# Kernel tuning notes

Hardware: AMD Instinct MI355X
Metric: run time of the kernel (lower is better)

The kernel has to match this reference:

```python
import jax, jax.numpy as jnp
from jax import lax
import numpy as np

B, H, W = 2, 48, 48
C_IN, C_OUT = 96, 192
D_INNER, N_STATE, DT_RANK, K = 192, 16, 6, 4  # VMamba: expand=2, d_state=16, dt_rank=ceil(C/16)
EPS = 1e-5


def setup_inputs() -> dict:
    ks = jax.random.split(jax.random.key(0), 16)
    s = 0.02
    r = lambda k, sh, sc=s: jax.random.normal(k, sh, jnp.float32) * sc
    d, N, R = D_INNER, N_STATE, DT_RANK
    return {
        "x": jax.random.normal(ks[0], (B, C_IN, H, W), jnp.float32),
        "ln_g": jnp.ones((C_IN,), jnp.float32),
        "ln_b": jnp.zeros((C_IN,), jnp.float32),
        "in_proj_w": r(ks[1], (2 * d, C_IN)),
        "dwconv_w": r(ks[2], (d, 1, 3, 3)),
        "dwconv_b": jnp.zeros((d,), jnp.float32),
        "x_proj_w": r(ks[3], (K, R + 2 * N, d)),
        "dt_w": r(ks[4], (K, d, R)),
        "dt_b": r(ks[5], (K, d), 0.1),
        "A_logs": jnp.tile(jnp.log(jnp.arange(1, N + 1, dtype=jnp.float32)), (K, d, 1)),
        "Ds": jnp.ones((K, d), jnp.float32),
        "out_norm_g": jnp.ones((d,), jnp.float32),
        "out_norm_b": jnp.zeros((d,), jnp.float32),
        "out_proj_w": r(ks[6], (C_IN, d)),
        "w1": r(ks[7], (C_OUT, C_IN, 1, 1)),
        "b1": jnp.zeros((C_OUT,), jnp.float32),
        "w31": r(ks[8], (C_OUT, C_IN, 3, 3)),
        "b31": jnp.zeros((C_OUT,), jnp.float32),
        "w32": r(ks[9], (C_OUT, C_IN, 3, 3)),
        "b32": jnp.zeros((C_OUT,), jnp.float32),
        "w33": r(ks[10], (C_OUT, C_OUT, 3, 3)),
        "b33": jnp.zeros((C_OUT,), jnp.float32),
        "bn_g": jnp.ones((3 * C_OUT,), jnp.float32),
        "bn_b": jnp.zeros((3 * C_OUT,), jnp.float32),
        "bn_m": r(ks[11], (3 * C_OUT,), 0.1),
        "bn_v": jax.random.uniform(ks[12], (3 * C_OUT,), jnp.float32) + 0.5,
        "prelu_a": jnp.float32(0.25),
    }


def _layernorm(x, g, b):
    m = jnp.mean(x, -1, keepdims=True)
    v = jnp.var(x, -1, keepdims=True)
    return (x - m) * lax.rsqrt(v + EPS) * g + b


def _conv(x, w, b, stride, pad, groups=1):
    y = lax.conv_general_dilated(x, w, (stride, stride), [(pad, pad), (pad, pad)],
                                 dimension_numbers=("NCHW", "OIHW", "NCHW"),
                                 feature_group_count=groups)
    return y + b[None, :, None, None]


def _ss2d(x, in_proj_w, dwconv_w, dwconv_b, x_proj_w, dt_w, dt_b, A_logs, Ds,
          out_norm_g, out_norm_b, out_proj_w):
    # x: (B, H, W, C)
    Bb, Hh, Ww, C = x.shape
    d, N, R = D_INNER, N_STATE, DT_RANK
    L = Hh * Ww
    xz = jnp.einsum("bhwc,ec->bhwe", x, in_proj_w)  # (B,H,W,2d)
    xin, z = jnp.split(xz, 2, axis=-1)
    xc = jnp.transpose(xin, (0, 3, 1, 2))           # (B,d,H,W)
    xc = jax.nn.silu(_conv(xc, dwconv_w, dwconv_b, 1, 1, groups=d))
    # 4 scan directions: row-major, col-major, and their reverses
    x_flat = xc.reshape(Bb, d, L)
    x_t = jnp.transpose(xc, (0, 1, 3, 2)).reshape(Bb, d, L)
    xs = jnp.stack([x_flat, x_t, x_flat[:, :, ::-1], x_t[:, :, ::-1]], axis=1)  # (B,K,d,L)
    x_dbl = jnp.einsum("bkdl,kcd->bkcl", xs, x_proj_w)
    dts, Bs, Cs = x_dbl[:, :, :R], x_dbl[:, :, R:R + N], x_dbl[:, :, R + N:]
    delta = jax.nn.softplus(jnp.einsum("bkrl,kdr->bkdl", dts, dt_w) + dt_b[None, :, :, None])
    A = -jnp.exp(A_logs)                                   # (K,d,N)
    dA = jnp.exp(jnp.einsum("bkdl,kdn->lbkdn", delta, A))  # (L,B,K,d,N)
    dBu = jnp.einsum("bkdl,bknl,bkdl->lbkdn", delta, Bs, xs)
    Cseq = jnp.transpose(Cs, (3, 0, 1, 2))                 # (L,B,K,N)

    def step(h, inp):
        dA_t, dBu_t, c_t = inp
        h = dA_t * h + dBu_t
        return h, jnp.einsum("bkdn,bkn->bkd", h, c_t)

    h0 = jnp.zeros((Bb, K, d, N), x.dtype)
    _, ys = lax.scan(step, h0, (dA, dBu, Cseq))            # ys: (L,B,K,d)
    ys = jnp.transpose(ys, (1, 2, 3, 0)) + xs * Ds[None, :, :, None]  # (B,K,d,L)

    def t_back(a):  # undo the HW transpose of col-major scans
        return jnp.transpose(a.reshape(Bb, d, Ww, Hh), (0, 1, 3, 2)).reshape(Bb, d, L)

    y = ys[:, 0] + ys[:, 2, :, ::-1] + t_back(ys[:, 1]) + t_back(ys[:, 3, :, ::-1])
    y = _layernorm(jnp.transpose(y, (0, 2, 1)), out_norm_g, out_norm_b).reshape(Bb, Hh, Ww, d)
    y = y * jax.nn.silu(z)
    return jnp.einsum("bhwd,cd->bhwc", y, out_proj_w)


def reference(x, ln_g, ln_b, in_proj_w, dwconv_w, dwconv_b, x_proj_w, dt_w, dt_b,
              A_logs, Ds, out_norm_g, out_norm_b, out_proj_w,
              w1, b1, w31, b31, w32, b32, w33, b33,
              bn_g, bn_b, bn_m, bn_v, prelu_a):
    # VSSBlock: residual + SS2D on LayerNorm'd NHWC features
    x_nhwc = jnp.transpose(x, (0, 2, 3, 1))
    x_nhwc = x_nhwc + _ss2d(_layernorm(x_nhwc, ln_g, ln_b), in_proj_w, dwconv_w,
                            dwconv_b, x_proj_w, dt_w, dt_b, A_logs, Ds,
                            out_norm_g, out_norm_b, out_proj_w)
    xm = jnp.transpose(x_nhwc, (0, 3, 1, 2))  # (B,C,H,W)
    # multi-branch stride-2 downsample
    x1 = _conv(xm, w1, b1, 2, 0)
    x2 = _conv(xm, w31, b31, 2, 1)
    x3 = _conv(_conv(xm, w32, b32, 2, 1), w33, b33, 1, 1)
    out = jnp.concatenate([x1, x2, x3], axis=1)  # (B, 3*C_OUT, H/2, W/2)
    # BatchNorm2d (inference, running stats) + PReLU(single param)
    out = (out - bn_m[None, :, None, None]) * lax.rsqrt(bn_v + EPS)[None, :, None, None] \
          * bn_g[None, :, None, None] + bn_b[None, :, None, None]
    return jnp.where(out > 0, out, prelu_a * out)
```

## Files before the change

### kernel.cpp

```cpp
#include <hip/hip_runtime.h>
#include <math.h>

#define BB_ 2
#define HH 48
#define WW 48
#define LL 2304
#define CIN 96
#define DD 192
#define KK 4
#define NN 16
#define RR 6
#define NCH 64
#define LC 36
#define COUT 192
#define OH 24
#define OW 24
#define OHW 576
#define NPX 1152
#define NTOT 4608
#define EPSF 1e-5f

__global__ __launch_bounds__(256) void k_prep(const float* __restrict__ x,
                                              const float* __restrict__ g,
                                              const float* __restrict__ b,
                                              const float* __restrict__ inw,
                                              const float* __restrict__ xpw,
                                              const float* __restrict__ w31,
                                              const float* __restrict__ w32,
                                              const float* __restrict__ w33,
                                              const float* __restrict__ w1,
                                              const float* __restrict__ wout,
                                              float* __restrict__ stats,
                                              float* __restrict__ WgT,
                                              float* __restrict__ sWg,
                                              float* __restrict__ sWb,
                                              float* __restrict__ At3,
                                              float* __restrict__ At1,
                                              float* __restrict__ At2,
                                              float* __restrict__ woutT) {
  int bx = blockIdx.x;
  int tid = threadIdx.x;
  if (bx < 72) {
    int bb = bx / 36; int l0 = (bx % 36) * 64;
    int p = tid >> 2, q = tid & 3;
    int l = l0 + p;
    const float* xp = x + bb * CIN * LL + l;
    float s = 0.f, ss = 0.f;
    for (int c = q; c < CIN; c += 4) { float v = xp[c * LL]; s += v; ss += v * v; }
    s += __shfl_xor(s, 1, 64); s += __shfl_xor(s, 2, 64);
    ss += __shfl_xor(ss, 1, 64); ss += __shfl_xor(ss, 2, 64);
    if (q == 0) {
      float m = s / CIN; float var = ss / CIN - m * m;
      stats[(bb * LL + l) * 2 + 0] = m;
      stats[(bb * LL + l) * 2 + 1] = rsqrtf(var + EPSF);
    }
  } else if (bx == 72) {
    for (int e = tid; e < 2 * DD; e += 256) {
      float swg = 0.f, swb = 0.f;
      for (int c = 0; c < CIN; c++) {
        float w = inw[e * CIN + c];
        float wg = w * g[c];
        WgT[c * 384 + e] = wg;
        swg += wg; swb += w * b[c];
      }
      sWg[e] = swg; sWb[e] = swb;
    }
  } else if (bx < 217) {
    int idx = (bx - 73) * 256 + tid;
    if (idx < 192 * 192) {
      int m = idx % 192, d = idx / 192;
      At3[idx] = (m < 152) ? xpw[m * 192 + d] : 0.f;
    }
  } else if (bx < 2161) {
    int i = (bx - 217) * 256 + tid;
    if (i < 864 * 576) {
      int k = i / 576, m = i % 576;
      float v;
      if (m < 192) v = w31[m * 864 + k];
      else if (m < 384) v = w32[(m - 192) * 864 + k];
      else v = (k % 9 == 4) ? w1[(m - 384) * 96 + k / 9] : 0.f;
      At1[i] = v;
    }
  } else if (bx < 3457) {
    int i = (bx - 2161) * 256 + tid;
    if (i < 1728 * 192) {
      int k = i / 192, m = i % 192;
      At2[i] = w33[m * 1728 + k];
    }
  } else {
    int i = (bx - 3457) * 256 + tid;
    if (i < 192 * 128) {
      int d = i / 128, e = i % 128;
      woutT[i] = (e < 96) ? wout[e * 192 + d] : 0.f;
    }
  }
}

__global__ __launch_bounds__(256) void k_dwconv(const float* __restrict__ xin,
                                                const float* __restrict__ wdw,
                                                const float* __restrict__ bdw,
                                                float* __restrict__ xs,
                                                float* __restrict__ xsl) {
  __shared__ float vt[32 * 50];
  int bid = blockIdx.x;
  int bb = bid / 288; int r = bid % 288; int dg = r / 72; int tile = r % 72;
  int l0 = tile * 32;
  int d0 = dg * 48;
  for (int i = threadIdx.x; i < 32 * 48; i += 256) {
    int lj = i & 31, dl = i >> 5;
    int d = d0 + dl;
    int l = l0 + lj;
    int h = l / WW, w = l % WW;
    const float* xp = xin + (bb * DD + d) * LL;
    const float* wq = wdw + d * 9;
    float acc = bdw[d];
#pragma unroll
    for (int kh = 0; kh < 3; kh++) {
      int ih = h + kh - 1; if (ih < 0 || ih >= HH) continue;
#pragma unroll
      for (int kw = 0; kw < 3; kw++) {
        int iw = w + kw - 1; if (iw < 0 || iw >= WW) continue;
        acc += xp[ih * WW + iw] * wq[kh * 3 + kw];
      }
    }
    float v = acc / (1.f + __expf(-acc));
    vt[lj * 50 + dl] = v;
    xsl[(size_t)d * NTOT + bb * LL + l] = v;
  }
  __syncthreads();
  for (int j = threadIdx.x; j < 32 * 48; j += 256) {
    int lj = j / 48, dl = j - lj * 48;
    int d = d0 + dl;
    int l = l0 + lj;
    int h = l / WW, w = l % WW;
    int lt = w * HH + h;
    float v = vt[lj * 50 + dl];
    xs[(((size_t)bb * KK + 0) * LL + l) * DD + d] = v;
    xs[(((size_t)bb * KK + 1) * LL + lt) * DD + d] = v;
    xs[(((size_t)bb * KK + 2) * LL + (LL - 1 - l)) * DD + d] = v;
    xs[(((size_t)bb * KK + 3) * LL + (LL - 1 - lt)) * DD + d] = v;
  }
}

__global__ __launch_bounds__(256) void k_dtsplit(const float* __restrict__ C1,
                                                 const float* __restrict__ dtw,
                                                 const float* __restrict__ dtb,
                                                 float* __restrict__ Bsb,
                                                 float* __restrict__ Csb,
                                                 float* __restrict__ delta) {
  __shared__ float lds[38 * 33];
  int bid = blockIdx.x;
  int tile = bid % 72; int bk = bid / 72; int bb = bk >> 2; int k = bk & 3;
  int l0 = tile * 32;
  int tid = threadIdx.x;
  for (int i = tid; i < 38 * 32; i += 256) {
    int r = i >> 5, lj = i & 31;
    lds[r * 33 + lj] = C1[(size_t)(k * 38 + r) * NTOT + bb * LL + l0 + lj];
  }
  __syncthreads();
  for (int i = tid; i < 32 * 16; i += 256) {
    int lj = i >> 4, n = i & 15;
    int l = l0 + lj; int h = l / WW, w = l % WW; int lt = w * HH + h;
    int pos = (k == 0) ? l : (k == 1) ? lt : (k == 2) ? (LL - 1 - l) : (LL - 1 - lt);
    size_t base = ((size_t)bk * LL + pos) * NN + n;
    Bsb[base] = lds[(6 + n) * 33 + lj];
    Csb[base] = lds[(22 + n) * 33 + lj];
  }
  for (int i = tid; i < 32 * 192; i += 256) {
    int lj = i / 192, d = i - lj * 192;
    int l = l0 + lj; int h = l / WW, w = l % WW; int lt = w * HH + h;
    int pos = (k == 0) ? l : (k == 1) ? lt : (k == 2) ? (LL - 1 - l) : (LL - 1 - lt);
    const float* wd = dtw + (k * DD + d) * RR;
    float acc = dtb[k * DD + d];
#pragma unroll
    for (int r = 0; r < RR; r++) acc += wd[r] * lds[r * 33 + lj];
    float sp = acc > 20.f ? acc : log1pf(__expf(acc));
    delta[((size_t)bk * LL + pos) * DD + d] = sp;
  }
}

__global__ __launch_bounds__(192) void k_scan1(const float* __restrict__ delta,
                                               const float* __restrict__ xs,
                                               const float* __restrict__ Bsb,
                                               const float* __restrict__ A_logs,
                                               float* __restrict__ Pbuf,
                                               float* __restrict__ Sbuf) {
  __shared__ float Bls[LC * NN];
  int bid = blockIdx.x;
  int c = bid & (NCH - 1); int bk = bid >> 6; int k = bk & 3;
  int t0 = c * LC;
  int d = threadIdx.x;
  const float* bp = Bsb + ((size_t)bk * LL + t0) * NN;
  for (int i = d; i < LC * NN; i += 192) Bls[i] = bp[i];
  float A[NN];
  {
    const float4* ap = (const float4*)(A_logs + (k * DD + d) * NN);
#pragma unroll
    for (int j = 0; j < 4; j++) {
      float4 a4 = ap[j];
      A[4 * j + 0] = -__expf(a4.x); A[4 * j + 1] = -__expf(a4.y);
      A[4 * j + 2] = -__expf(a4.z); A[4 * j + 3] = -__expf(a4.w);
    }
  }
  bool seq = true;
#pragma unroll
  for (int n = 0; n < NN; n++) seq = seq && (fabsf(A[n] + (float)(n + 1)) < 1e-3f);
  float h[NN];
#pragma unroll
  for (int n = 0; n < NN; n++) h[n] = 0.f;
  float sd = 0.f;
  __syncthreads();
  const float* dp = delta + ((size_t)bk * LL + t0) * DD + d;
  const float* xp = xs + ((size_t)bk * LL + t0) * DD + d;
#pragma unroll 2
  for (int t = 0; t < LC; ++t) {
    float dt = dp[t * DD];
    float xv = xp[t * DD];
    float u = dt * xv;
    sd += dt;
    float dA[NN];
    if (seq) {
      float q = __expf(-dt);
      dA[0] = q;
#pragma unroll
      for (int n = 1; n < NN; n++) dA[n] = dA[n - 1] * q;
    } else {
#pragma unroll
      for (int n = 0; n < NN; n++) dA[n] = __expf(dt * A[n]);
    }
    const float4* b4 = (const float4*)&Bls[t * NN];
#pragma unroll
    for (int j = 0; j < 4; j++) {
      float4 bv = b4[j];
      h[4 * j + 0] = dA[4 * j + 0] * h[4 * j + 0] + u * bv.x;
      h[4 * j + 1] = dA[4 * j + 1] * h[4 * j + 1] + u * bv.y;
      h[4 * j + 2] = dA[4 * j + 2] * h[4 * j + 2] + u * bv.z;
      h[4 * j + 3] = dA[4 * j + 3] * h[4 * j + 3] + u * bv.w;
    }
  }
  int chn = (bk * DD + d) * NN;
  float* pp = Pbuf + (size_t)c * 24576 + chn;
  float* sp = Sbuf + (size_t)c * 24576 + chn;
#pragma unroll
  for (int n = 0; n < NN; n++) { pp[n] = __expf(A[n] * sd); sp[n] = h[n]; }
}

__global__ __launch_bounds__(256) void k_scan2(const float* __restrict__ Pbuf,
                                               const float* __restrict__ Sbuf,
                                               float* __restrict__ Hinit) {
  int idx = blockIdx.x * 256 + threadIdx.x;
  float h = 0.f;
  for (int c = 0; c < NCH; c++) {
    Hinit[(size_t)c * 24576 + idx] = h;
    h = Pbuf[(size_t)c * 24576 + idx] * h + Sbuf[(size_t)c * 24576 + idx];
  }
}

__global__ __launch_bounds__(192) void k_scan3(const float* __restrict__ delta,
                                               const float* __restrict__ xs,
                                               const float* __restrict__ Bsb,
                                               const float* __restrict__ Csb,
                                               const float* __restrict__ A_logs,
                                               const float* __restrict__ Ds,
                                               const float* __restrict__ Hinit,
                                               float* __restrict__ ys) {
  __shared__ float Bls[LC * NN];
  __shared__ float Cls[LC * NN];
  int bid = blockIdx.x;
  int c = bid & (NCH - 1); int bk = bid >> 6; int k = bk & 3;
  int t0 = c * LC;
  int d = threadIdx.x;
  const float* bp = Bsb + ((size_t)bk * LL + t0) * NN;
  const float* cp = Csb + ((size_t)bk * LL + t0) * NN;
  for (int i = d; i < LC * NN; i += 192) { Bls[i] = bp[i]; Cls[i] = cp[i]; }
  float A[NN];
  {
    const float4* ap = (const float4*)(A_logs + (k * DD + d) * NN);
#pragma unroll
    for (int j = 0; j < 4; j++) {
      float4 a4 = ap[j];
      A[4 * j + 0] = -__expf(a4.x); A[4 * j + 1] = -__expf(a4.y);
      A[4 * j + 2] = -__expf(a4.z); A[4 * j + 3] = -__expf(a4.w);
    }
  }
  bool seq = true;
#pragma unroll
  for (int n = 0; n < NN; n++) seq = seq && (fabsf(A[n] + (float)(n + 1)) < 1e-3f);
  float Dv = Ds[k * DD + d];
  float h[NN];
  {
    const float4* hp = (const float4*)(Hinit + (size_t)c * 24576 + (bk * DD + d) * NN);
#pragma unroll
    for (int j = 0; j < 4; j++) {
      float4 h4 = hp[j];
      h[4 * j + 0] = h4.x; h[4 * j + 1] = h4.y;
      h[4 * j + 2] = h4.z; h[4 * j + 3] = h4.w;
    }
  }
  __syncthreads();
  const float* dp = delta + ((size_t)bk * LL + t0) * DD + d;
  const float* xp = xs + ((size_t)bk * LL + t0) * DD + d;
  float* yp = ys + ((size_t)bk * LL + t0) * DD + d;
#pragma unroll 2
  for (int t = 0; t < LC; ++t) {
    float dt = dp[t * DD];
    float xv = xp[t * DD];
    float u = dt * xv;
    float y = 0.f;
    float dA[NN];
    if (seq) {
      float q = __expf(-dt);
      dA[0] = q;
#pragma unroll
      for (int n = 1; n < NN; n++) dA[n] = dA[n - 1] * q;
    } else {
#pragma unroll
      for (int n = 0; n < NN; n++) dA[n] = __expf(dt * A[n]);
    }
    const float4* b4 = (const float4*)&Bls[t * NN];
    const float4* c4 = (const float4*)&Cls[t * NN];
#pragma unroll
    for (int j = 0; j < 4; j++) {
      float4 bv = b4[j];
      float4 cc = c4[j];
      h[4 * j + 0] = dA[4 * j + 0] * h[4 * j + 0] + u * bv.x;
      h[4 * j + 1] = dA[4 * j + 1] * h[4 * j + 1] + u * bv.y;
      h[4 * j + 2] = dA[4 * j + 2] * h[4 * j + 2] + u * bv.z;
      h[4 * j + 3] = dA[4 * j + 3] * h[4 * j + 3] + u * bv.w;
      y += h[4 * j + 0] * cc.x + h[4 * j + 1] * cc.y
         + h[4 * j + 2] * cc.z + h[4 * j + 3] * cc.w;
    }
    yp[t * DD] = y + Dv * xv;
  }
}

__global__ __launch_bounds__(256) void k_combine(const float* __restrict__ ys,
                                                 const float* __restrict__ z,
                                                 const float* __restrict__ ong,
                                                 const float* __restrict__ onb,
                                                 float* __restrict__ ya) {
  __shared__ float yt[32 * 193];
  int bx = blockIdx.x; int bb = bx / 72; int l0 = (bx % 72) * 32;
  int tid = threadIdx.x;
  for (int i = tid; i < 32 * DD; i += 256) {
    int p = i / DD, d = i - p * DD;
    int l = l0 + p; int h = l / WW, w = l - h * WW;
    int t1 = w * HH + h;
    float v = ys[(((size_t)bb * KK + 0) * LL + l) * DD + d]
            + ys[(((size_t)bb * KK + 1) * LL + t1) * DD + d]
            + ys[(((size_t)bb * KK + 2) * LL + (LL - 1 - l)) * DD + d]
            + ys[(((size_t)bb * KK + 3) * LL + (LL - 1 - t1)) * DD + d];
    yt[p * 193 + d] = v;
  }
  __syncthreads();
  int p = tid >> 3, q = tid & 7;
  int l = l0 + p;
  float s = 0.f, ss = 0.f;
  for (int d = q * 24; d < q * 24 + 24; d++) { float v = yt[p * 193 + d]; s += v; ss += v * v; }
  s += __shfl_xor(s, 1, 64); s += __shfl_xor(s, 2, 64); s += __shfl_xor(s, 4, 64);
  ss += __shfl_xor(ss, 1, 64); ss += __shfl_xor(ss, 2, 64); ss += __shfl_xor(ss, 4, 64);
  float m = s / DD, var = ss / DD - m * m;
  float rr = rsqrtf(var + EPSF);
  const float* zp = z + (bb * LL + l) * DD;
  for (int d = q * 24; d < q * 24 + 24; d++) {
    float v = (yt[p * 193 + d] - m) * rr * ong[d] + onb[d];
    float zv = zp[d];
    yt[p * 193 + d] = v * zv / (1.f + __expf(-zv));
  }
  __syncthreads();
  for (int i = tid; i < 32 * DD; i += 256) {
    int d = i >> 5, p2 = i & 31;
    ya[(bb * DD + d) * LL + l0 + p2] = yt[p2 * 193 + d];
  }
}

__global__ __launch_bounds__(256) void k_pack1(const float* __restrict__ xm,
                                               float* __restrict__ Bm1) {
  int idx4 = blockIdx.x * 256 + threadIdx.x;
  if (idx4 >= 864 * 288) return;
  int k = idx4 / 288; int n = (idx4 % 288) * 4;
  int ci = k / 9, r9 = k % 9, kh = r9 / 3, kw = r9 % 3;
  int bb = n / OHW, rem = n % OHW, oh = rem / OW, ow0 = rem % OW;
  int ih = 2 * oh + kh - 1;
  float4 v = {0.f, 0.f, 0.f, 0.f};
  if (ih >= 0 && ih < HH) {
    const float* base = xm + (bb * CIN + ci) * LL + ih * WW;
    int iw0 = 2 * ow0 + kw - 1;
    v.x = (iw0 >= 0) ? base[iw0] : 0.f;
    v.y = base[iw0 + 2];
    v.z = base[iw0 + 4];
    v.w = base[iw0 + 6];
  }
  *(float4*)&Bm1[k * NPX + n] = v;
}

__global__ __launch_bounds__(256) void k_pack2(const float* __restrict__ t3,
                                               float* __restrict__ Bm2) {
  int idx4 = blockIdx.x * 256 + threadIdx.x;
  if (idx4 >= 1728 * 288) return;
  int k = idx4 / 288; int n = (idx4 % 288) * 4;
  int ci = k / 9, r9 = k % 9, kh = r9 / 3, kw = r9 % 3;
  int bb = n / OHW, rem = n % OHW, oh = rem / OW, ow0 = rem % OW;
  int ih = oh + kh - 1;
  float4 v = {0.f, 0.f, 0.f, 0.f};
  if (ih >= 0 && ih < OH) {
    const float* base = t3 + (bb * COUT + ci) * OHW + ih * OW;
    int iw0 = ow0 + kw - 1;
    v.x = (iw0 >= 0) ? base[iw0] : 0.f;
    v.y = base[iw0 + 1];
    v.z = base[iw0 + 2];
    v.w = (iw0 + 3 < OW) ? base[iw0 + 3] : 0.f;
  }
  *(float4*)&Bm2[k * NPX + n] = v;
}

template<int MT, int KCHUNK, int NB>
__global__ __launch_bounds__(256) void k_gemm(const float* __restrict__ At,
                                              const float* __restrict__ Bm,
                                              float* __restrict__ Cout) {
  __shared__ float As[16][64];
  __shared__ float Bs[16][64];
  int n0 = blockIdx.x * 64;
  int m0 = blockIdx.y * 64;
  int kz = blockIdx.z;
  int k0 = kz * KCHUNK;
  int tid = threadIdx.x;
  int lr = tid >> 4;
  int lc = (tid & 15) * 4;
  int tm = tid >> 4;
  int tn = tid & 15;
  float acc[4][4] = {};
  for (int ks = 0; ks < KCHUNK; ks += 16) {
    int kg = k0 + ks + lr;
    *(float4*)&As[lr][lc] = *(const float4*)&At[kg * MT + m0 + lc];
    *(float4*)&Bs[lr][lc] = *(const float4*)&Bm[(size_t)kg * NB + n0 + lc];
    __syncthreads();
#pragma unroll
    for (int kk = 0; kk < 16; kk++) {
      float4 a = *(float4*)&As[kk][tm * 4];
      float4 b = *(float4*)&Bs[kk][tn * 4];
      acc[0][0] += a.x * b.x; acc[0][1] += a.x * b.y; acc[0][2] += a.x * b.z; acc[0][3] += a.x * b.w;
      acc[1][0] += a.y * b.x; acc[1][1] += a.y * b.y; acc[1][2] += a.y * b.z; acc[1][3] += a.y * b.w;
      acc[2][0] += a.z * b.x; acc[2][1] += a.z * b.y; acc[2][2] += a.z * b.z; acc[2][3] += a.z * b.w;
      acc[3][0] += a.w * b.x; acc[3][1] += a.w * b.y; acc[3][2] += a.w * b.z; acc[3][3] += a.w * b.w;
    }
    __syncthreads();
  }
  float* cp = Cout + ((size_t)kz * MT + m0) * NB + n0;
#pragma unroll
  for (int i = 0; i < 4; i++) {
    float4 v = {acc[i][0], acc[i][1], acc[i][2], acc[i][3]};
    *(float4*)&cp[(size_t)(tm * 4 + i) * NB + tn * 4] = v;
  }
}

template<int MT, int KD, int EPI>
__global__ __launch_bounds__(256) void k_gemmF(const float* __restrict__ At,
                                               const float* __restrict__ Bm,
                                               int ldb, int boffB,
                                               float* __restrict__ C0,
                                               int ldc, int boffC,
                                               const float* __restrict__ a0,
                                               const float* __restrict__ a1,
                                               const float* __restrict__ a2,
                                               float* __restrict__ a3) {
  __shared__ float As[16][64];
  __shared__ float Bs[16][64];
  int n0 = blockIdx.x * 64;
  int m0 = blockIdx.y * 64;
  int bb = blockIdx.z;
  const float* B = Bm + (size_t)bb * boffB;
  int tid = threadIdx.x;
  int lr = tid >> 4;
  int lc = (tid & 15) * 4;
  int tm = tid >> 4;
  int tn = tid & 15;
  float acc[4][4] = {};
  for (int ks = 0; ks < KD; ks += 16) {
    *(float4*)&As[lr][lc] = *(const float4*)&At[(ks + lr) * MT + m0 + lc];
    *(float4*)&Bs[lr][lc] = *(const float4*)&B[(size_t)(ks + lr) * ldb + n0 + lc];
    __syncthreads();
#pragma unroll
    for (int kk = 0; kk < 16; kk++) {
      float4 a = *(float4*)&As[kk][tm * 4];
      float4 b = *(float4*)&Bs[kk][tn * 4];
      acc[0][0] += a.x * b.x; acc[0][1] += a.x * b.y; acc[0][2] += a.x * b.z; acc[0][3] += a.x * b.w;
      acc[1][0] += a.y * b.x; acc[1][1] += a.y * b.y; acc[1][2] += a.y * b.z; acc[1][3] += a.y * b.w;
      acc[2][0] += a.z * b.x; acc[2][1] += a.z * b.y; acc[2][2] += a.z * b.z; acc[2][3] += a.z * b.w;
      acc[3][0] += a.w * b.x; acc[3][1] += a.w * b.y; acc[3][2] += a.w * b.z; acc[3][3] += a.w * b.w;
    }
    __syncthreads();
  }
  int n = n0 + tn * 4;
  if (EPI == 2) {
    float m_[4], r_[4];
#pragma unroll
    for (int j = 0; j < 4; j++) {
      m_[j] = a0[((size_t)bb * LL + n + j) * 2];
      r_[j] = a0[((size_t)bb * LL + n + j) * 2 + 1];
    }
#pragma unroll
    for (int i = 0; i < 4; i++) {
      int e = m0 + tm * 4 + i;
      float swg = a1[e], swb = a2[e];
      float v0 = r_[0] * (acc[i][0] - m_[0] * swg) + swb;
      float v1 = r_[1] * (acc[i][1] - m_[1] * swg) + swb;
      float v2 = r_[2] * (acc[i][2] - m_[2] * swg) + swb;
      float v3 = r_[3] * (acc[i][3] - m_[3] * swg) + swb;
      if (e < DD) {
        float4 v = {v0, v1, v2, v3};
        *(float4*)&C0[(size_t)bb * boffC + (size_t)e * ldc + n] = v;
      } else {
        a3[((size_t)bb * LL + n + 0) * DD + (e - DD)] = v0;
        a3[((size_t)bb * LL + n + 1) * DD + (e - DD)] = v1;
        a3[((size_t)bb * LL + n + 2) * DD + (e - DD)] = v2;
        a3[((size_t)bb * LL + n + 3) * DD + (e - DD)] = v3;
      }
    }
  } else {
#pragma unroll
    for (int i = 0; i < 4; i++) {
      int e = m0 + tm * 4 + i;
      if (e < CIN) {
        size_t off = (size_t)bb * boffC + (size_t)e * ldc + n;
        float4 xr = *(const float4*)&a0[off];
        float4 v = {acc[i][0] + xr.x, acc[i][1] + xr.y, acc[i][2] + xr.z, acc[i][3] + xr.w};
        *(float4*)&C0[off] = v;
      }
    }
  }
}

__global__ __launch_bounds__(256) void k_reduce1(const float* __restrict__ Cp1,
                                                 const float* __restrict__ b1,
                                                 const float* __restrict__ b31,
                                                 const float* __restrict__ b32,
                                                 const float* __restrict__ bn_g,
                                                 const float* __restrict__ bn_b,
                                                 const float* __restrict__ bn_m,
                                                 const float* __restrict__ bn_v,
                                                 const float* __restrict__ prelu_a,
                                                 float* __restrict__ out,
                                                 float* __restrict__ t3) {
  int idx = blockIdx.x * 256 + threadIdx.x;
  if (idx >= 576 * NPX) return;
  int m = idx / NPX, n = idx % NPX;
  float s = 0.f;
#pragma unroll
  for (int c = 0; c < 6; c++) s += Cp1[(size_t)c * 576 * NPX + idx];
  int bb = n / OHW, o = n % OHW;
  if (m < 192) {
    s += b31[m];
    int cc = 192 + m;
    float scale = rsqrtf(bn_v[cc] + EPSF) * bn_g[cc];
    float v = s * scale + (bn_b[cc] - bn_m[cc] * scale);
    float a = prelu_a[0];
    out[((size_t)bb * 576 + cc) * OHW + o] = v > 0.f ? v : a * v;
  } else if (m < 384) {
    s += b32[m - 192];
    t3[((size_t)bb * COUT + (m - 192)) * OHW + o] = s;
  } else {
    s += b1[m - 384];
    int cc = m - 384;
    float scale = rsqrtf(bn_v[cc] + EPSF) * bn_g[cc];
    float v = s * scale + (bn_b[cc] - bn_m[cc] * scale);
    float a = prelu_a[0];
    out[((size_t)bb * 576 + cc) * OHW + o] = v > 0.f ? v : a * v;
  }
}

__global__ __launch_bounds__(256) void k_reduce2(const float* __restrict__ Cp2,
                                                 const float* __restrict__ b33,
                                                 const float* __restrict__ bn_g,
                                                 const float* __restrict__ bn_b,
                                                 const float* __restrict__ bn_m,
                                                 const float* __restrict__ bn_v,
                                                 const float* __restrict__ prelu_a,
                                                 float* __restrict__ out) {
  int idx = blockIdx.x * 256 + threadIdx.x;
  if (idx >= 192 * NPX) return;
  int m = idx / NPX, n = idx % NPX;
  float s = b33[m];
#pragma unroll
  for (int c = 0; c < 9; c++) s += Cp2[(size_t)c * 192 * NPX + idx];
  int bb = n / OHW, o = n % OHW;
  int cc = 384 + m;
  float scale = rsqrtf(bn_v[cc] + EPSF) * bn_g[cc];
  float v = s * scale + (bn_b[cc] - bn_m[cc] * scale);
  float a = prelu_a[0];
  out[((size_t)bb * 576 + cc) * OHW + o] = v > 0.f ? v : a * v;
}

extern "C" void kernel_launch(void* const* d_in, const int* in_sizes, int n_in,
                              void* d_out, int out_size, void* d_ws, size_t ws_size,
                              hipStream_t stream) {
  const float* x        = (const float*)d_in[0];
  const float* ln_g     = (const float*)d_in[1];
  const float* ln_b     = (const float*)d_in[2];
  const float* in_proj_w= (const float*)d_in[3];
  const float* dwconv_w = (const float*)d_in[4];
  const float* dwconv_b = (const float*)d_in[5];
  const float* x_proj_w = (const float*)d_in[6];
  const float* dt_w     = (const float*)d_in[7];
  const float* dt_b     = (const float*)d_in[8];
  const float* A_logs   = (const float*)d_in[9];
  const float* Ds       = (const float*)d_in[10];
  const float* out_norm_g = (const float*)d_in[11];
  const float* out_norm_b = (const float*)d_in[12];
  const float* out_proj_w = (const float*)d_in[13];
  const float* w1  = (const float*)d_in[14];
  const float* b1  = (const float*)d_in[15];
  const float* w31 = (const float*)d_in[16];
  const float* b31 = (const float*)d_in[17];
  const float* w32 = (const float*)d_in[18];
  const float* b32 = (const float*)d_in[19];
  const float* w33 = (const float*)d_in[20];
  const float* b33 = (const float*)d_in[21];
  const float* bn_g = (const float*)d_in[22];
  const float* bn_b = (const float*)d_in[23];
  const float* bn_m = (const float*)d_in[24];
  const float* bn_v = (const float*)d_in[25];
  const float* prelu_a = (const float*)d_in[26];

  float* ws = (float*)d_ws;
  float* stats = ws + 0;
  float* WgT   = ws + 16384;
  float* sWg   = ws + 65536;
  float* sWb   = ws + 66048;
  float* At3   = ws + 98304;
  float* At1   = ws + 147456;
  float* At2   = ws + 655360;
  float* woutT = ws + 1048576;
  float* xin   = ws + 2097152;
  float* z     = ws + 3145728;
  float* xs    = ws + 4194304;
  float* xsl   = ws + 8388608;
  float* C1    = ws + 9437184;
  float* delta = ws + 10485760;
  float* Bsb   = ws + 14155776;
  float* Csb   = ws + 14680064;
  float* Pbuf  = ws + 15728640;
  float* Sbuf  = ws + 17301504;
  float* Hinit = ws + 18874368;
  float* ys    = ws + 20971520;
  float* ya    = ws + 25165824;
  float* xm    = ws + 26214400;
  float* t3    = ws + 27262976;
  float* Bm1   = ws + 28311552;
  float* Bm2   = ws + 29360128;
  float* Cp1   = ws + 31457280;
  float* Cp2   = ws + 35651584;
  float* out = (float*)d_out;

  k_prep<<<3553, 256, 0, stream>>>(x, ln_g, ln_b, in_proj_w, x_proj_w,
                                   w31, w32, w33, w1, out_proj_w,
                                   stats, WgT, sWg, sWb, At3, At1, At2, woutT);
  k_gemmF<384, 96, 2><<<dim3(36, 6, 2), 256, 0, stream>>>(
      WgT, x, LL, CIN * LL, xin, LL, DD * LL, stats, sWg, sWb, z);
  k_dwconv<<<576, 256, 0, stream>>>(xin, dwconv_w, dwconv_b, xs, xsl);
  k_gemm<192, 192, NTOT><<<dim3(72, 3, 1), 256, 0, stream>>>(At3, xsl, C1);
  k_dtsplit<<<576, 256, 0, stream>>>(C1, dt_w, dt_b, Bsb, Csb, delta);
  k_scan1<<<512, 192, 0, stream>>>(delta, xs, Bsb, A_logs, Pbuf, Sbuf);
  k_scan2<<<96, 256, 0, stream>>>(Pbuf, Sbuf, Hinit);
  k_scan3<<<512, 192, 0, stream>>>(delta, xs, Bsb, Csb, A_logs, Ds, Hinit, ys);
  k_combine<<<144, 256, 0, stream>>>(ys, z, out_norm_g, out_norm_b, ya);
  k_gemmF<128, 192, 3><<<dim3(36, 2, 2), 256, 0, stream>>>(
      woutT, ya, LL, DD * LL, xm, LL, CIN * LL, x, nullptr, nullptr, nullptr);
  k_pack1<<<972, 256, 0, stream>>>(xm, Bm1);
  k_gemm<576, 144, NPX><<<dim3(18, 9, 6), 256, 0, stream>>>(At1, Bm1, Cp1);
  k_reduce1<<<2592, 256, 0, stream>>>(Cp1, b1, b31, b32, bn_g, bn_b, bn_m, bn_v,
                                      prelu_a, out, t3);
  k_pack2<<<1944, 256, 0, stream>>>(t3, Bm2);
  k_gemm<192, 192, NPX><<<dim3(18, 3, 9), 256, 0, stream>>>(At2, Bm2, Cp2);
  k_reduce2<<<864, 256, 0, stream>>>(Cp2, b33, bn_g, bn_b, bn_m, bn_v, prelu_a, out);
}
```

Baseline: 205.9 us.

## Fuse im2col into conv GEMMs, tile weight transposes, dedupe scan inputs

The explicit im2col pack kernels are removed. The conv GEMMs now gather input patches straight from the feature maps while loading their B tiles, which saves two launches and a large staging buffer round trip. The weight transposes in the prep kernel now go through shared-memory 32x32 tiles so both reads and writes are coalesced. The dwconv kernel stores only two scan-direction copies of xs instead of four, and the scans read the reversed directions with a negative stride. The cost is uncoalesced, bounds-checked gathers inside the GEMM inner loop.

```diff
diff --git a/kernel.cpp b/kernel.cpp
--- a/kernel.cpp
+++ b/kernel.cpp
@@ -38,6 +38,7 @@
                                               float* __restrict__ At1,
                                               float* __restrict__ At2,
                                               float* __restrict__ woutT) {
+  __shared__ float tile[32][33];
   int bx = blockIdx.x;
   int tid = threadIdx.x;
   if (bx < 72) {
@@ -65,30 +66,41 @@
       }
       sWg[e] = swg; sWb[e] = swb;
     }
-  } else if (bx < 217) {
+  } else if (bx < 218) {
     int idx = (bx - 73) * 256 + tid;
     if (idx < 192 * 192) {
       int m = idx % 192, d = idx / 192;
       At3[idx] = (m < 152) ? xpw[m * 192 + d] : 0.f;
     }
-  } else if (bx < 2161) {
-    int i = (bx - 217) * 256 + tid;
-    if (i < 864 * 576) {
-      int k = i / 576, m = i % 576;
-      float v;
-      if (m < 192) v = w31[m * 864 + k];
-      else if (m < 384) v = w32[(m - 192) * 864 + k];
-      else v = (k % 9 == 4) ? w1[(m - 384) * 96 + k / 9] : 0.f;
-      At1[i] = v;
-    }
-  } else if (bx < 3457) {
-    int i = (bx - 2161) * 256 + tid;
-    if (i < 1728 * 192) {
+  } else if (bx < 542) {
+    int tt = bx - 218;
+    const float* srcw = (tt < 162) ? w31 : w32;
+    int mofs = (tt < 162) ? 0 : 192;
+    if (tt >= 162) tt -= 162;
+    int kt = tt / 6, mt = tt % 6;
+    int r = tid >> 5, c = tid & 31;
+    for (int rr = r; rr < 32; rr += 8)
+      tile[rr][c] = srcw[(mt * 32 + rr) * 864 + kt * 32 + c];
+    __syncthreads();
+    for (int rr = r; rr < 32; rr += 8)
+      At1[(kt * 32 + rr) * 576 + mofs + mt * 32 + c] = tile[c][rr];
+  } else if (bx < 1190) {
+    int i = (bx - 542) * 256 + tid;
+    if (i < 864 * 192) {
       int k = i / 192, m = i % 192;
-      At2[i] = w33[m * 1728 + k];
-    }
+      At1[k * 576 + 384 + m] = (k % 9 == 4) ? w1[m * 96 + k / 9] : 0.f;
+    }
+  } else if (bx < 1514) {
+    int tt = bx - 1190;
+    int kt = tt / 6, mt = tt % 6;
+    int r = tid >> 5, c = tid & 31;
+    for (int rr = r; rr < 32; rr += 8)
+      tile[rr][c] = w33[(mt * 32 + rr) * 1728 + kt * 32 + c];
+    __syncthreads();
+    for (int rr = r; rr < 32; rr += 8)
+      At2[(kt * 32 + rr) * 192 + mt * 32 + c] = tile[c][rr];
   } else {
-    int i = (bx - 3457) * 256 + tid;
+    int i = (bx - 1514) * 256 + tid;
     if (i < 192 * 128) {
       int d = i / 128, e = i % 128;
       woutT[i] = (e < 96) ? wout[e * 192 + d] : 0.f;
@@ -135,10 +147,8 @@
     int h = l / WW, w = l % WW;
     int lt = w * HH + h;
     float v = vt[lj * 50 + dl];
-    xs[(((size_t)bb * KK + 0) * LL + l) * DD + d] = v;
-    xs[(((size_t)bb * KK + 1) * LL + lt) * DD + d] = v;
-    xs[(((size_t)bb * KK + 2) * LL + (LL - 1 - l)) * DD + d] = v;
-    xs[(((size_t)bb * KK + 3) * LL + (LL - 1 - lt)) * DD + d] = v;
+    xs[((size_t)(bb * 2 + 0) * LL + l) * DD + d] = v;
+    xs[((size_t)(bb * 2 + 1) * LL + lt) * DD + d] = v;
   }
 }
 
@@ -187,7 +197,7 @@
                                                float* __restrict__ Sbuf) {
   __shared__ float Bls[LC * NN];
   int bid = blockIdx.x;
-  int c = bid & (NCH - 1); int bk = bid >> 6; int k = bk & 3;
+  int c = bid & (NCH - 1); int bk = bid >> 6; int k = bk & 3; int bb = bk >> 2;
   int t0 = c * LC;
   int d = threadIdx.x;
   const float* bp = Bsb + ((size_t)bk * LL + t0) * NN;
@@ -211,11 +221,14 @@
   float sd = 0.f;
   __syncthreads();
   const float* dp = delta + ((size_t)bk * LL + t0) * DD + d;
-  const float* xp = xs + ((size_t)bk * LL + t0) * DD + d;
+  const float* xpb = xs + ((size_t)(bb * 2 + (k & 1)) * LL) * DD + d;
+  const float* xp; int xstep;
+  if (k < 2) { xp = xpb + (size_t)t0 * DD; xstep = DD; }
+  else       { xp = xpb + (size_t)(LL - 1 - t0) * DD; xstep = -DD; }
 #pragma unroll 2
   for (int t = 0; t < LC; ++t) {
     float dt = dp[t * DD];
-    float xv = xp[t * DD];
+    float xv = xp[t * xstep];
     float u = dt * xv;
     sd += dt;
     float dA[NN];
@@ -267,7 +280,7 @@
   __shared__ float Bls[LC * NN];
   __shared__ float Cls[LC * NN];
   int bid = blockIdx.x;
-  int c = bid & (NCH - 1); int bk = bid >> 6; int k = bk & 3;
+  int c = bid & (NCH - 1); int bk = bid >> 6; int k = bk & 3; int bb = bk >> 2;
   int t0 = c * LC;
   int d = threadIdx.x;
   const float* bp = Bsb + ((size_t)bk * LL + t0) * NN;
@@ -299,12 +312,15 @@
   }
   __syncthreads();
   const float* dp = delta + ((size_t)bk * LL + t0) * DD + d;
-  const float* xp = xs + ((size_t)bk * LL + t0) * DD + d;
+  const float* xpb = xs + ((size_t)(bb * 2 + (k & 1)) * LL) * DD + d;
+  const float* xp; int xstep;
+  if (k < 2) { xp = xpb + (size_t)t0 * DD; xstep = DD; }
+  else       { xp = xpb + (size_t)(LL - 1 - t0) * DD; xstep = -DD; }
   float* yp = ys + ((size_t)bk * LL + t0) * DD + d;
 #pragma unroll 2
   for (int t = 0; t < LC; ++t) {
     float dt = dp[t * DD];
-    float xv = xp[t * DD];
+    float xv = xp[t * xstep];
     float u = dt * xv;
     float y = 0.f;
     float dA[NN];
@@ -372,46 +388,6 @@
     int d = i >> 5, p2 = i & 31;
     ya[(bb * DD + d) * LL + l0 + p2] = yt[p2 * 193 + d];
   }
-}
-
-__global__ __launch_bounds__(256) void k_pack1(const float* __restrict__ xm,
-                                               float* __restrict__ Bm1) {
-  int idx4 = blockIdx.x * 256 + threadIdx.x;
-  if (idx4 >= 864 * 288) return;
-  int k = idx4 / 288; int n = (idx4 % 288) * 4;
-  int ci = k / 9, r9 = k % 9, kh = r9 / 3, kw = r9 % 3;
-  int bb = n / OHW, rem = n % OHW, oh = rem / OW, ow0 = rem % OW;
-  int ih = 2 * oh + kh - 1;
-  float4 v = {0.f, 0.f, 0.f, 0.f};
-  if (ih >= 0 && ih < HH) {
-    const float* base = xm + (bb * CIN + ci) * LL + ih * WW;
-    int iw0 = 2 * ow0 + kw - 1;
-    v.x = (iw0 >= 0) ? base[iw0] : 0.f;
-    v.y = base[iw0 + 2];
-    v.z = base[iw0 + 4];
-    v.w = base[iw0 + 6];
-  }
-  *(float4*)&Bm1[k * NPX + n] = v;
-}
-
-__global__ __launch_bounds__(256) void k_pack2(const float* __restrict__ t3,
-                                               float* __restrict__ Bm2) {
-  int idx4 = blockIdx.x * 256 + threadIdx.x;
-  if (idx4 >= 1728 * 288) return;
-  int k = idx4 / 288; int n = (idx4 % 288) * 4;
-  int ci = k / 9, r9 = k % 9, kh = r9 / 3, kw = r9 % 3;
-  int bb = n / OHW, rem = n % OHW, oh = rem / OW, ow0 = rem % OW;
-  int ih = oh + kh - 1;
-  float4 v = {0.f, 0.f, 0.f, 0.f};
-  if (ih >= 0 && ih < OH) {
-    const float* base = t3 + (bb * COUT + ci) * OHW + ih * OW;
-    int iw0 = ow0 + kw - 1;
-    v.x = (iw0 >= 0) ? base[iw0] : 0.f;
-    v.y = base[iw0 + 1];
-    v.z = base[iw0 + 2];
-    v.w = (iw0 + 3 < OW) ? base[iw0 + 3] : 0.f;
-  }
-  *(float4*)&Bm2[k * NPX + n] = v;
 }
 
 template<int MT, int KCHUNK, int NB>
@@ -451,6 +427,61 @@
   for (int i = 0; i < 4; i++) {
     float4 v = {acc[i][0], acc[i][1], acc[i][2], acc[i][3]};
     *(float4*)&cp[(size_t)(tm * 4 + i) * NB + tn * 4] = v;
+  }
+}
+
+template<int MT, int KCHUNK, int CI, int IH, int STRIDE>
+__global__ __launch_bounds__(256) void k_cgemm(const float* __restrict__ At,
+                                               const float* __restrict__ SRC,
+                                               float* __restrict__ Cout) {
+  __shared__ float As[16][64];
+  __shared__ float Bs[16][64];
+  int n0 = blockIdx.x * 64;
+  int m0 = blockIdx.y * 64;
+  int kz = blockIdx.z;
+  int k0 = kz * KCHUNK;
+  int tid = threadIdx.x;
+  int lr = tid >> 4;
+  int lc = (tid & 15) * 4;
+  int tm = tid >> 4;
+  int tn = tid & 15;
+  int n = n0 + lc;
+  int bb = n / OHW;
+  int rem = n - bb * OHW;
+  int oh = rem / OW, ow0 = rem - oh * OW;
+  float acc[4][4] = {};
+  for (int ks = 0; ks < KCHUNK; ks += 16) {
+    int kg = k0 + ks + lr;
+    int ci = kg / 9, r9 = kg - ci * 9;
+    int kh = r9 / 3, kw = r9 - kh * 3;
+    int ih = STRIDE * oh + kh - 1;
+    const float* src = SRC + ((size_t)(bb * CI + ci)) * (IH * IH) + ih * IH;
+    float bvv[4];
+#pragma unroll
+    for (int j = 0; j < 4; j++) {
+      int iw = STRIDE * (ow0 + j) + kw - 1;
+      bvv[j] = (ih >= 0 && ih < IH && iw >= 0 && iw < IH) ? src[iw] : 0.f;
+    }
+    float4 bv = {bvv[0], bvv[1], bvv[2], bvv[3]};
+    *(float4*)&Bs[lr][lc] = bv;
+    *(float4*)&As[lr][lc] = *(const float4*)&At[kg * MT + m0 + lc];
+    __syncthreads();
+#pragma unroll
+    for (int kk = 0; kk < 16; kk++) {
+      float4 a = *(float4*)&As[kk][tm * 4];
+      float4 b = *(float4*)&Bs[kk][tn * 4];
+      acc[0][0] += a.x * b.x; acc[0][1] += a.x * b.y; acc[0][2] += a.x * b.z; acc[0][3] += a.x * b.w;
+      acc[1][0] += a.y * b.x; acc[1][1] += a.y * b.y; acc[1][2] += a.y * b.z; acc[1][3] += a.y * b.w;
+      acc[2][0] += a.z * b.x; acc[2][1] += a.z * b.y; acc[2][2] += a.z * b.z; acc[2][3] += a.z * b.w;
+      acc[3][0] += a.w * b.x; acc[3][1] += a.w * b.y; acc[3][2] += a.w * b.z; acc[3][3] += a.w * b.w;
+    }
+    __syncthreads();
+  }
+  float* cp = Cout + ((size_t)kz * MT + m0) * NPX + n0;
+#pragma unroll
+  for (int i = 0; i < 4; i++) {
+    float4 v = {acc[i][0], acc[i][1], acc[i][2], acc[i][3]};
+    *(float4*)&cp[(size_t)(tm * 4 + i) * NPX + tn * 4] = v;
   }
 }
 
@@ -646,13 +677,11 @@
   float* ya    = ws + 25165824;
   float* xm    = ws + 26214400;
   float* t3    = ws + 27262976;
-  float* Bm1   = ws + 28311552;
-  float* Bm2   = ws + 29360128;
   float* Cp1   = ws + 31457280;
   float* Cp2   = ws + 35651584;
   float* out = (float*)d_out;
 
-  k_prep<<<3553, 256, 0, stream>>>(x, ln_g, ln_b, in_proj_w, x_proj_w,
+  k_prep<<<1610, 256, 0, stream>>>(x, ln_g, ln_b, in_proj_w, x_proj_w,
                                    w31, w32, w33, w1, out_proj_w,
                                    stats, WgT, sWg, sWb, At3, At1, At2, woutT);
   k_gemmF<384, 96, 2><<<dim3(36, 6, 2), 256, 0, stream>>>(
@@ -666,11 +695,9 @@
   k_combine<<<144, 256, 0, stream>>>(ys, z, out_norm_g, out_norm_b, ya);
   k_gemmF<128, 192, 3><<<dim3(36, 2, 2), 256, 0, stream>>>(
       woutT, ya, LL, DD * LL, xm, LL, CIN * LL, x, nullptr, nullptr, nullptr);
-  k_pack1<<<972, 256, 0, stream>>>(xm, Bm1);
-  k_gemm<576, 144, NPX><<<dim3(18, 9, 6), 256, 0, stream>>>(At1, Bm1, Cp1);
+  k_cgemm<576, 144, CIN, HH, 2><<<dim3(18, 9, 6), 256, 0, stream>>>(At1, xm, Cp1);
   k_reduce1<<<2592, 256, 0, stream>>>(Cp1, b1, b31, b32, bn_g, bn_b, bn_m, bn_v,
                                       prelu_a, out, t3);
-  k_pack2<<<1944, 256, 0, stream>>>(t3, Bm2);
-  k_gemm<192, 192, NPX><<<dim3(18, 3, 9), 256, 0, stream>>>(At2, Bm2, Cp2);
+  k_cgemm<192, 192, COUT, OH, 1><<<dim3(18, 3, 9), 256, 0, stream>>>(At2, t3, Cp2);
   k_reduce2<<<864, 256, 0, stream>>>(Cp2, b33, bn_g, bn_b, bn_m, bn_v, prelu_a, out);
 }
```

Result: no change. 204.6 us (-0.6%).
